# Kernel tuning notes

Measured on AMD Instinct MI355X. Metric: run time of the kernel, lower is better.

The kernel has to match this reference:

```python
import jax, jax.numpy as jnp
import numpy as np

C = 19
D = 128
TAU_HARD = 0.2
EMA = 0.999
BETA = 0.7
TH_I, TH_F = 0.5, 0.85
TL_I, TL_F = 0.1, 0.3
EPS = 1e-7


def _l2norm(x, axis):
    n = jnp.linalg.norm(x, axis=axis, keepdims=True)
    return x / jnp.maximum(n, 1e-12)


def _flatten_feat(feat):
    # [B,D,Hf,Wf] -> [N,D]
    B, Dd, Hf, Wf = feat.shape
    return feat.transpose(0, 2, 3, 1).reshape(-1, Dd)


def _build_protos(feat, labels, weights=None):
    # single-pass segment reduce replacing the per-class python loop
    f = _flatten_feat(feat)
    seg = labels.reshape(-1)
    w = jnp.ones(seg.shape, f.dtype) if weights is None else weights.reshape(-1)
    wsum_f = jax.ops.segment_sum(w[:, None] * f, seg, num_segments=C)  # [C,D]
    wsum = jax.ops.segment_sum(w, seg, num_segments=C)                 # [C]
    cnt = jax.ops.segment_sum(jnp.ones_like(w), seg, num_segments=C)
    proto = wsum_f / (wsum[:, None] + EPS)
    return proto, cnt >= 1.0


def _hard_contrastive(feat, labels, mem, mem_init):
    f = _l2norm(_flatten_feat(feat), axis=1)          # [N,D]
    lab = labels.reshape(-1)
    valid = mem_init[lab].astype(f.dtype)
    logits = (f @ mem.T) / TAU_HARD                   # [N,C]
    ce = -jnp.take_along_axis(jax.nn.log_softmax(logits, axis=1), lab[:, None], axis=1)[:, 0]
    nv = jnp.sum(valid)
    return jnp.where(nv > 0, jnp.sum(ce * valid) / jnp.maximum(nv, 1.0), 0.0)


def _ce_map(logits, target):
    # per-pixel cross entropy, logits [B,C,H,W], target [B,H,W]
    ls = jax.nn.log_softmax(logits, axis=1)
    return -jnp.take_along_axis(ls, target[:, None], axis=1)[:, 0]


def setup_inputs() -> dict:
    key = jax.random.key(0)
    ks = jax.random.split(key, 9)
    B, Hf, Wf = 4, 128, 128
    H = W = 512
    f = lambda k: jax.random.normal(k, (B, D, Hf, Wf), jnp.float32)
    g = lambda k: jax.random.normal(k, (B, C, H, W), jnp.float32)
    return {
        "feat_l1": f(ks[0]), "feat_l2": f(ks[1]),
        "feat_u1": f(ks[2]), "feat_u2": f(ks[3]),
        "logits_l1": g(ks[4]), "logits_l2": g(ks[5]),
        "logits_u1": g(ks[6]), "logits_u2": g(ks[7]),
        "memory": jnp.zeros((C, D), jnp.float32),
        "gt_labels": jax.random.randint(ks[8], (B, H, W), 0, C),
        "memory_init": jnp.zeros((C,), bool),
        "cur_iter": 10000,
        "max_iter": 40000,
    }


def reference(feat_l1, feat_l2, feat_u1, feat_u2, logits_l1, logits_l2,
              logits_u1, logits_u2, memory, gt_labels, memory_init,
              cur_iter, max_iter):
    B, _, Hf, Wf = feat_l1.shape
    H, W = logits_u1.shape[2], logits_u1.shape[3]

    q_u1 = jax.nn.softmax(logits_u1, axis=1)
    q_u2 = jax.nn.softmax(logits_u2, axis=1)

    # reliability r_u [B,H,W]
    y1 = jnp.argmax(q_u1, axis=1)
    y2 = jnp.argmax(q_u2, axis=1)
    agree = (y1 == y2).astype(q_u1.dtype)
    conf = (jnp.max(q_u1, axis=1) + jnp.max(q_u2, axis=1)) / 2.0
    m = (q_u1 + q_u2) / 2.0
    logm = jnp.log(jnp.maximum(m, EPS))
    kl1 = jnp.sum(q_u1 * (jnp.log(jnp.maximum(q_u1, EPS)) - logm), axis=1)
    kl2 = jnp.sum(q_u2 * (jnp.log(jnp.maximum(q_u2, EPS)) - logm), axis=1)
    r_u = agree * conf * jnp.exp(-(kl1 + kl2) / 2.0)

    # cosine-annealed thresholds
    ratio = float(cur_iter) / max(int(max_iter), 1)
    tau_high = TH_F - (TH_F - TH_I) * np.cos(np.pi * ratio / 2)

    # UCPS (pseudo labels are argmax of logits == argmax of softmax)
    loss_ucps = jnp.mean(jax.lax.stop_gradient(r_u) * (_ce_map(logits_u1, y2) + _ce_map(logits_u2, y1)))

    # nearest downsample (integer stride, matches torch nearest floor indexing)
    ih = jnp.arange(Hf) * (H // Hf)
    iw = jnp.arange(Wf) * (W // Wf)
    gt_down = gt_labels[:, ih][:, :, iw]
    pseudo_consensus = jnp.where(y1 != y2, 0, y1)
    pseudo_u_down = pseudo_consensus[:, ih][:, :, iw]
    # bilinear (align_corners=False == half-pixel, no antialias)
    r_u_down = jax.image.resize(r_u, (B, Hf, Wf), method='linear', antialias=False)

    anchor_mask = r_u_down > tau_high

    feat_l = (feat_l1 + feat_l2) / 2.0
    feat_u = (feat_u1 + feat_u2) / 2.0
    pl, pl_pres = _build_protos(feat_l, gt_down)
    anchor_r = jnp.where(anchor_mask, r_u_down, 0.0)
    pu, pu_pres = _build_protos(feat_u, pseudo_u_down, anchor_r)

    both = pl_pres & pu_pres
    merged = jnp.where(both[:, None], BETA * pl + (1.0 - BETA) * pu,
                       jnp.where(pl_pres[:, None], pl, pu))
    present = pl_pres | pu_pres
    merged = jax.lax.stop_gradient(merged)  # update_memory is no_grad

    p_norm = _l2norm(merged, axis=1)
    ema = _l2norm(EMA * memory + (1.0 - EMA) * p_norm, axis=1)
    new_mem = jnp.where((present & ~memory_init)[:, None], p_norm,
                        jnp.where((present & memory_init)[:, None], ema, memory))
    new_init = memory_init | present
    new_mem = jax.lax.stop_gradient(new_mem)

    loss_hard_l = (_hard_contrastive(feat_l1, gt_down, new_mem, new_init)
                   + _hard_contrastive(feat_l2, gt_down, new_mem, new_init)) / 2.0
    # contrastive_mode == 'all_hard'
    loss_hard_u = (_hard_contrastive(feat_u1, pseudo_u_down, new_mem, new_init)
                   + _hard_contrastive(feat_u2, pseudo_u_down, new_mem, new_init)) / 2.0

    loss_dgpc = loss_hard_l + loss_hard_u  # loss_soft == 0 in all_hard mode
    return jnp.stack([loss_dgpc, loss_ucps])
```

## Files before the change

kernel.cpp:

```cpp
#include <hip/hip_runtime.h>
#include <math.h>

#define NCLS 19
#define DD   128
#define EPSV 1e-7f
#define LOGEPS -16.118095651f

#define OFF_TAU    0
#define OFF_CNTL   8
#define OFF_WSUMU  32
#define OFF_CNTU   64
#define OFF_CE     96
#define OFF_VALID  100
#define OFF_UCPS   104
#define OFF_SUML   128
#define OFF_SUMU   2560
#define OFF_MEM    4992
#define OFF_INIT   7424
#define OFF_RUD    7456
#define OFF_PSEUDO 72992
#define ZERO_N     72992

__device__ __forceinline__ void fatom(float* p, float v) { unsafeAtomicAdd(p, v); }

__global__ __launch_bounds__(256) void kZ(float* __restrict__ W,
                                          const int* __restrict__ cur_it,
                                          const int* __restrict__ max_it) {
    int i = blockIdx.x * 256 + threadIdx.x;
    if (i == 0) {
        int mi = max_it[0]; if (mi < 1) mi = 1;
        double ratio = (double)cur_it[0] / (double)mi;
        W[OFF_TAU] = (float)(0.85 - (0.85 - 0.5) * cos(M_PI * ratio * 0.5));
    } else if (i < ZERO_N) {
        W[i] = 0.0f;
    }
}

__global__ __launch_bounds__(256, 2) void kB(const float* __restrict__ lu1,
                                             const float* __restrict__ lu2,
                                             float* __restrict__ W) {
    float* rud = W + OFF_RUD;
    int* pseudo = (int*)(W + OFF_PSEUDO);
    int t = blockIdx.x * 256 + threadIdx.x;
    int b = t >> 16;
    int rem4 = (t << 2) & 262143;
    int h = rem4 >> 9, w0 = rem4 & 511;

    const float4* p1 = (const float4*)lu1 + (size_t)b * (NCLS * 65536) + (rem4 >> 2);
    const float4* p2 = (const float4*)lu2 + (size_t)b * (NCLS * 65536) + (rem4 >> 2);

    float4 v1[NCLS], v2[NCLS];
#pragma unroll
    for (int c = 0; c < NCLS; c++) v1[c] = p1[c * 65536];
#pragma unroll
    for (int c = 0; c < NCLS; c++) v2[c] = p2[c * 65536];
    const float* a1 = (const float*)v1;
    const float* a2 = (const float*)v2;

    float contrib = 0.f;
    float ru12 = 0.f;
    int pl0 = 0;

#pragma unroll
    for (int e = 0; e < 4; e++) {
        float m1 = a1[e]; int y1 = 0;
        float m2 = a2[e]; int y2 = 0;
#pragma unroll
        for (int c = 1; c < NCLS; c++) {
            float x1 = a1[c * 4 + e], x2 = a2[c * 4 + e];
            if (x1 > m1) { m1 = x1; y1 = c; }
            if (x2 > m2) { m2 = x2; y2 = c; }
        }
        float s1 = 0.f, s2 = 0.f;
#pragma unroll
        for (int c = 0; c < NCLS; c++) {
            s1 += __expf(a1[c * 4 + e] - m1);
            s2 += __expf(a2[c * 4 + e] - m2);
        }
        float lse1 = m1 + __logf(s1);
        float lse2 = m2 + __logf(s2);

        float kl = 0.f, l1y2 = a1[e], l2y1 = a2[e];
#pragma unroll
        for (int c = 0; c < NCLS; c++) {
            float x1 = a1[c * 4 + e], x2 = a2[c * 4 + e];
            float lq1 = x1 - lse1, lq2 = x2 - lse2;
            float q1 = __expf(lq1), q2 = __expf(lq2);
            float mm = 0.5f * (q1 + q2);
            float lm = __logf(fmaxf(mm, EPSV));
            kl += q1 * (fmaxf(lq1, LOGEPS) - lm) + q2 * (fmaxf(lq2, LOGEPS) - lm);
            if (c == y2) l1y2 = x1;
            if (c == y1) l2y1 = x2;
        }
        float conf = 0.5f * (1.f / s1 + 1.f / s2);
        float r_u = (y1 == y2) ? conf * __expf(-0.5f * kl) : 0.f;
        float ce = (lse1 - l1y2) + (lse2 - l2y1);
        contrib += r_u * ce;
        if (e == 1 || e == 2) ru12 += r_u;
        if (e == 0) pl0 = (y1 == y2) ? y1 : 0;
    }

    float cs = contrib;
#pragma unroll
    for (int o = 32; o > 0; o >>= 1) cs += __shfl_down(cs, o, 64);
    __shared__ float wsum[4];
    if ((threadIdx.x & 63) == 0) wsum[threadIdx.x >> 6] = cs;
    __syncthreads();
    if (threadIdx.x == 0) fatom(&W[OFF_UCPS], wsum[0] + wsum[1] + wsum[2] + wsum[3]);

    int hm = h & 3;
    int didx = b * 16384 + (h >> 2) * 128 + (w0 >> 2);
    if (hm == 1 || hm == 2) fatom(&rud[didx], 0.25f * ru12);
    if (hm == 0) pseudo[didx] = pl0;
}

__global__ __launch_bounds__(256) void kC(const float* __restrict__ fl1,
                                          const float* __restrict__ fl2,
                                          const float* __restrict__ fu1,
                                          const float* __restrict__ fu2,
                                          const int* __restrict__ gt,
                                          float* __restrict__ W) {
    __shared__ float tile[DD * 33];
    __shared__ float accL[2 * NCLS * DD];
    __shared__ int   sLab[32], sCu[32];
    __shared__ float sW[32];
    __shared__ float sCntL[NCLS], sCntU[NCLS], sWUs[NCLS];

    int tid = threadIdx.x;
    for (int i = tid; i < 2 * NCLS * DD; i += 256) accL[i] = 0.f;
    if (tid < NCLS) { sCntL[tid] = 0.f; sCntU[tid] = 0.f; sWUs[tid] = 0.f; }
    __syncthreads();

    int P0 = blockIdx.x * 128;
    int b = P0 >> 14;
    const float tau = W[OFF_TAU];
    const float* rud = W + OFF_RUD;
    const int* pseudo = (const int*)(W + OFF_PSEUDO);
    size_t gb = (size_t)b * 2097152;

    int d = tid & 127, pg = tid >> 7;

    for (int T = 0; T < 4; T++) {
        int rem0 = (P0 + T * 32) & 16383;
        if (tid < 32) {
            int rem = rem0 + tid;
            int bp = b * 16384 + rem;
            int ii = rem >> 7, jj = rem & 127;
            int cl = gt[b * 262144 + ii * 2048 + jj * 4];
            int cu = pseudo[bp];
            float rd = rud[bp];
            float w = (rd > tau) ? rd : 0.f;
            sLab[tid] = cl; sCu[tid] = cu; sW[tid] = w;
            fatom(&sCntL[cl], 1.f);
            fatom(&sCntU[cu], 1.f);
            if (w > 0.f) fatom(&sWUs[cu], w);
        }
        for (int i = tid; i < 1024; i += 256) {
            int dd = i >> 3, p4 = (i & 7) << 2;
            size_t g = gb + (size_t)dd * 16384 + rem0 + p4;
            float4 x1 = *(const float4*)(fl1 + g);
            float4 x2 = *(const float4*)(fl2 + g);
            float* tp = &tile[dd * 33 + p4];
            tp[0] = 0.5f * (x1.x + x2.x);
            tp[1] = 0.5f * (x1.y + x2.y);
            tp[2] = 0.5f * (x1.z + x2.z);
            tp[3] = 0.5f * (x1.w + x2.w);
        }
        __syncthreads();
        float* aL = &accL[pg * (NCLS * DD) + d];
#pragma unroll
        for (int p = pg * 16; p < pg * 16 + 16; p++) {
            int c = sLab[p];
            aL[c * DD] += tile[d * 33 + p];
            float w = sW[p];
            if (w > 0.f) {
                size_t g = gb + (size_t)d * 16384 + rem0 + p;
                fatom(&W[OFF_SUMU + sCu[p] * DD + d], w * 0.5f * (fu1[g] + fu2[g]));
            }
        }
        __syncthreads();
    }
    for (int i = tid; i < NCLS * DD; i += 256)
        fatom(&W[OFF_SUML + i], accL[i] + accL[NCLS * DD + i]);
    if (tid < NCLS) {
        fatom(&W[OFF_CNTL + tid], sCntL[tid]);
        fatom(&W[OFF_WSUMU + tid], sWUs[tid]);
        fatom(&W[OFF_CNTU + tid], sCntU[tid]);
    }
}

__global__ __launch_bounds__(128) void kD(const float* __restrict__ mem,
                                          const unsigned char* __restrict__ minit,
                                          float* __restrict__ W) {
    int c = blockIdx.x, d = threadIdx.x;
    __shared__ float red[128];
    float cntL = W[OFF_CNTL + c], wsU = W[OFF_WSUMU + c], cntU = W[OFF_CNTU + c];
    bool plp = cntL >= 1.f, pup = cntU >= 1.f;
    float pl = W[OFF_SUML + c * DD + d] / (cntL + EPSV);
    float pu = W[OFF_SUMU + c * DD + d] / (wsU + EPSV);
    float merged = (plp && pup) ? (0.7f * pl + 0.3f * pu) : (plp ? pl : pu);

    red[d] = merged * merged; __syncthreads();
    for (int s = 64; s > 0; s >>= 1) { if (d < s) red[d] += red[d + s]; __syncthreads(); }
    float nrm = red[0];
    __syncthreads();
    float pn = merged / fmaxf(sqrtf(nrm), 1e-12f);

    float mo = mem[c * DD + d];
    float e = 0.999f * mo + 0.001f * pn;
    red[d] = e * e; __syncthreads();
    for (int s = 64; s > 0; s >>= 1) { if (d < s) red[d] += red[d + s]; __syncthreads(); }
    float ne = red[0];
    float ema = e / fmaxf(sqrtf(ne), 1e-12f);

    bool present = plp || pup;
    bool init = (minit[c] != 0);
    float nm = present ? (init ? ema : pn) : mo;
    W[OFF_MEM + c * DD + d] = nm;
    if (d == 0) W[OFF_INIT + c] = (init || present) ? 1.f : 0.f;
}

__device__ __forceinline__ void pix_loss(const float dots[NCLS], float nn, int lab,
                                         const float* sInit, float& ce_acc, float& v_acc) {
    float inv = 5.0f / fmaxf(sqrtf(nn), 1e-12f);
    float lg[NCLS];
#pragma unroll
    for (int c = 0; c < NCLS; c++) lg[c] = dots[c] * inv;
    float mx = lg[0];
#pragma unroll
    for (int c = 1; c < NCLS; c++) mx = fmaxf(mx, lg[c]);
    float s = 0.f;
#pragma unroll
    for (int c = 0; c < NCLS; c++) s += __expf(lg[c] - mx);
    float lse = mx + __logf(s);
    float ll = lg[0];
#pragma unroll
    for (int c = 1; c < NCLS; c++) if (c == lab) ll = lg[c];
    float vld = sInit[lab];
    ce_acc += vld * (lse - ll);
    v_acc += vld;
}

__global__ __launch_bounds__(256) void kE(const float* __restrict__ f0,
                                          const float* __restrict__ f1,
                                          const float* __restrict__ f2,
                                          const float* __restrict__ f3,
                                          const int* __restrict__ gt,
                                          float* __restrict__ W) {
    __shared__ __align__(16) float sMem[NCLS * DD];
    __shared__ float sInit[NCLS];
    __shared__ float redA[256], redB[256];
    int fid = blockIdx.y;
    const float* feat = (fid == 0) ? f0 : (fid == 1) ? f1 : (fid == 2) ? f2 : f3;
    for (int i = threadIdx.x; i < NCLS * DD; i += 256) sMem[i] = W[OFF_MEM + i];
    if (threadIdx.x < NCLS) sInit[threadIdx.x] = W[OFF_INIT + threadIdx.x];
    __syncthreads();

    int p0 = blockIdx.x * 512 + threadIdx.x;
    int b = p0 >> 14;
    int rem0 = p0 & 16383;
    const float* fp = feat + (size_t)b * 2097152 + rem0;

    float dots0[NCLS], dots1[NCLS];
#pragma unroll
    for (int c = 0; c < NCLS; c++) { dots0[c] = 0.f; dots1[c] = 0.f; }
    float n0 = 0.f, n1 = 0.f;

    for (int d0 = 0; d0 < DD; d0 += 8) {
        const float* fpp = fp + (size_t)d0 * 16384;
        float a[8], bb[8];
#pragma unroll
        for (int j = 0; j < 8; j++) {
            a[j]  = fpp[(size_t)j * 16384];
            bb[j] = fpp[(size_t)j * 16384 + 256];
        }
#pragma unroll
        for (int j = 0; j < 8; j++) { n0 += a[j] * a[j]; n1 += bb[j] * bb[j]; }
#pragma unroll
        for (int c = 0; c < NCLS; c++) {
            float4 m0 = *(const float4*)&sMem[c * DD + d0];
            float4 m1 = *(const float4*)&sMem[c * DD + d0 + 4];
            dots0[c] += a[0] * m0.x + a[1] * m0.y + a[2] * m0.z + a[3] * m0.w
                      + a[4] * m1.x + a[5] * m1.y + a[6] * m1.z + a[7] * m1.w;
            dots1[c] += bb[0] * m0.x + bb[1] * m0.y + bb[2] * m0.z + bb[3] * m0.w
                      + bb[4] * m1.x + bb[5] * m1.y + bb[6] * m1.z + bb[7] * m1.w;
        }
    }

    const int* pseudo = (const int*)(W + OFF_PSEUDO);
    int rem1 = rem0 + 256;
    int lab0 = (fid < 2) ? gt[b * 262144 + (rem0 >> 7) * 2048 + (rem0 & 127) * 4] : pseudo[p0];
    int lab1 = (fid < 2) ? gt[b * 262144 + (rem1 >> 7) * 2048 + (rem1 & 127) * 4] : pseudo[p0 + 256];

    float ce_acc = 0.f, v_acc = 0.f;
    pix_loss(dots0, n0, lab0, sInit, ce_acc, v_acc);
    pix_loss(dots1, n1, lab1, sInit, ce_acc, v_acc);

    redA[threadIdx.x] = ce_acc;
    redB[threadIdx.x] = v_acc;
    __syncthreads();
    for (int s = 128; s > 0; s >>= 1) {
        if (threadIdx.x < s) { redA[threadIdx.x] += redA[threadIdx.x + s]; redB[threadIdx.x] += redB[threadIdx.x + s]; }
        __syncthreads();
    }
    if (threadIdx.x == 0) {
        fatom(&W[OFF_CE + fid], redA[0]);
        fatom(&W[OFF_VALID + fid], redB[0]);
    }
}

__global__ void kF(float* __restrict__ out, const float* __restrict__ W) {
    if (threadIdx.x == 0 && blockIdx.x == 0) {
        float h[4];
#pragma unroll
        for (int i = 0; i < 4; i++) {
            float nv = W[OFF_VALID + i];
            h[i] = (nv > 0.f) ? W[OFF_CE + i] / fmaxf(nv, 1.f) : 0.f;
        }
        out[0] = 0.5f * (h[0] + h[1]) + 0.5f * (h[2] + h[3]);
        out[1] = W[OFF_UCPS] * (1.0f / 1048576.0f);
    }
}

extern "C" void kernel_launch(void* const* d_in, const int* in_sizes, int n_in,
                              void* d_out, int out_size, void* d_ws, size_t ws_size,
                              hipStream_t stream) {
    const float* fl1 = (const float*)d_in[0];
    const float* fl2 = (const float*)d_in[1];
    const float* fu1 = (const float*)d_in[2];
    const float* fu2 = (const float*)d_in[3];
    const float* lu1 = (const float*)d_in[6];
    const float* lu2 = (const float*)d_in[7];
    const float* mem = (const float*)d_in[8];
    const int* gt = (const int*)d_in[9];
    const unsigned char* minit = (const unsigned char*)d_in[10];
    const int* cur = (const int*)d_in[11];
    const int* mxi = (const int*)d_in[12];
    float* W = (float*)d_ws;
    float* out = (float*)d_out;

    kZ<<<286, 256, 0, stream>>>(W, cur, mxi);
    kB<<<1024, 256, 0, stream>>>(lu1, lu2, W);
    kC<<<512, 256, 0, stream>>>(fl1, fl2, fu1, fu2, gt, W);
    kD<<<NCLS, 128, 0, stream>>>(mem, minit, W);
    kE<<<dim3(128, 4), 256, 0, stream>>>(fl1, fl2, fu1, fu2, gt, W);
    kF<<<1, 64, 0, stream>>>(out, W);
}
```

Baseline: 418.1 us.

## Stage unsupervised logits through LDS and process one pixel per thread

```diff
diff --git a/kernel.cpp b/kernel.cpp
--- a/kernel.cpp
+++ b/kernel.cpp
@@ -36,82 +36,76 @@
     }
 }
 
-__global__ __launch_bounds__(256, 2) void kB(const float* __restrict__ lu1,
-                                             const float* __restrict__ lu2,
-                                             float* __restrict__ W) {
+__global__ __launch_bounds__(256) void kB(const float* __restrict__ lu1,
+                                          const float* __restrict__ lu2,
+                                          float* __restrict__ W) {
+    __shared__ float sA[NCLS * 256];
+    __shared__ float sB[NCLS * 256];
+    __shared__ float wsum[4];
+
     float* rud = W + OFF_RUD;
     int* pseudo = (int*)(W + OFF_PSEUDO);
-    int t = blockIdx.x * 256 + threadIdx.x;
-    int b = t >> 16;
-    int rem4 = (t << 2) & 262143;
-    int h = rem4 >> 9, w0 = rem4 & 511;
-
-    const float4* p1 = (const float4*)lu1 + (size_t)b * (NCLS * 65536) + (rem4 >> 2);
-    const float4* p2 = (const float4*)lu2 + (size_t)b * (NCLS * 65536) + (rem4 >> 2);
-
-    float4 v1[NCLS], v2[NCLS];
-#pragma unroll
-    for (int c = 0; c < NCLS; c++) v1[c] = p1[c * 65536];
-#pragma unroll
-    for (int c = 0; c < NCLS; c++) v2[c] = p2[c * 65536];
-    const float* a1 = (const float*)v1;
-    const float* a2 = (const float*)v2;
-
-    float contrib = 0.f;
-    float ru12 = 0.f;
-    int pl0 = 0;
-
-#pragma unroll
-    for (int e = 0; e < 4; e++) {
-        float m1 = a1[e]; int y1 = 0;
-        float m2 = a2[e]; int y2 = 0;
-#pragma unroll
-        for (int c = 1; c < NCLS; c++) {
-            float x1 = a1[c * 4 + e], x2 = a2[c * 4 + e];
-            if (x1 > m1) { m1 = x1; y1 = c; }
-            if (x2 > m2) { m2 = x2; y2 = c; }
-        }
-        float s1 = 0.f, s2 = 0.f;
-#pragma unroll
-        for (int c = 0; c < NCLS; c++) {
-            s1 += __expf(a1[c * 4 + e] - m1);
-            s2 += __expf(a2[c * 4 + e] - m2);
-        }
-        float lse1 = m1 + __logf(s1);
-        float lse2 = m2 + __logf(s2);
-
-        float kl = 0.f, l1y2 = a1[e], l2y1 = a2[e];
-#pragma unroll
-        for (int c = 0; c < NCLS; c++) {
-            float x1 = a1[c * 4 + e], x2 = a2[c * 4 + e];
-            float lq1 = x1 - lse1, lq2 = x2 - lse2;
-            float q1 = __expf(lq1), q2 = __expf(lq2);
-            float mm = 0.5f * (q1 + q2);
-            float lm = __logf(fmaxf(mm, EPSV));
-            kl += q1 * (fmaxf(lq1, LOGEPS) - lm) + q2 * (fmaxf(lq2, LOGEPS) - lm);
-            if (c == y2) l1y2 = x1;
-            if (c == y1) l2y1 = x2;
-        }
-        float conf = 0.5f * (1.f / s1 + 1.f / s2);
-        float r_u = (y1 == y2) ? conf * __expf(-0.5f * kl) : 0.f;
-        float ce = (lse1 - l1y2) + (lse2 - l2y1);
-        contrib += r_u * ce;
-        if (e == 1 || e == 2) ru12 += r_u;
-        if (e == 0) pl0 = (y1 == y2) ? y1 : 0;
-    }
-
-    float cs = contrib;
-#pragma unroll
-    for (int o = 32; o > 0; o >>= 1) cs += __shfl_down(cs, o, 64);
-    __shared__ float wsum[4];
-    if ((threadIdx.x & 63) == 0) wsum[threadIdx.x >> 6] = cs;
-    __syncthreads();
-    if (threadIdx.x == 0) fatom(&W[OFF_UCPS], wsum[0] + wsum[1] + wsum[2] + wsum[3]);
-
-    int hm = h & 3;
-    int didx = b * 16384 + (h >> 2) * 128 + (w0 >> 2);
-    if (hm == 1 || hm == 2) fatom(&rud[didx], 0.25f * ru12);
-    if (hm == 0) pseudo[didx] = pl0;
+    int tid = threadIdx.x;
+    int b = blockIdx.x >> 10;
+    int rem_base = (blockIdx.x & 1023) << 8;
+
+    {
+        const float4* g1 = (const float4*)lu1 + (size_t)b * (NCLS * 65536) + (rem_base >> 2);
+        const float4* g2 = (const float4*)lu2 + (size_t)b * (NCLS * 65536) + (rem_base >> 2);
+        float4* d1 = (float4*)sA;
+        float4* d2 = (float4*)sB;
+        for (int i = tid; i < NCLS * 64; i += 256) {
+            int c = i >> 6, e = i & 63;
+            d1[c * 64 + e] = g1[c * 65536 + e];
+            d2[c * 64 + e] = g2[c * 65536 + e];
+        }
+    }
+    __syncthreads();
+
+    float m1, m2, l1y2, l2y1;
+    int y1 = 0, y2 = 0;
+    m1 = sA[tid]; m2 = sB[tid];
+    l2y1 = m2;    l1y2 = m1;
+#pragma unroll
+    for (int c = 1; c < NCLS; c++) {
+        float x1 = sA[c * 256 + tid], x2 = sB[c * 256 + tid];
+        if (x1 > m1) { m1 = x1; y1 = c; l2y1 = x2; }
+        if (x2 > m2) { m2 = x2; y2 = c; l1y2 = x1; }
+    }
+    float s1 = 0.f, s2 = 0.f;
+#pragma unroll
+    for (int c = 0; c < NCLS; c++) {
+        s1 += __expf(sA[c * 256 + tid] - m1);
+        s2 += __expf(sB[c * 256 + tid] - m2);
+    }
+    float lse1 = m1 + __logf(s1);
+    float lse2 = m2 + __logf(s2);
+    float kl = 0.f;
+#pragma unroll
+    for (int c = 0; c < NCLS; c++) {
+        float lq1 = sA[c * 256 + tid] - lse1, lq2 = sB[c * 256 + tid] - lse2;
+        float q1 = __expf(lq1), q2 = __expf(lq2);
+        float mm = 0.5f * (q1 + q2);
+        float lm = __logf(fmaxf(mm, EPSV));
+        kl += q1 * (fmaxf(lq1, LOGEPS) - lm) + q2 * (fmaxf(lq2, LOGEPS) - lm);
+    }
+    float conf = 0.5f * (1.f / s1 + 1.f / s2);
+    float r_u = (y1 == y2) ? conf * __expf(-0.5f * kl) : 0.f;
+    float ce = (lse1 - l1y2) + (lse2 - l2y1);
+    float contrib = r_u * ce;
+
+#pragma unroll
+    for (int o = 32; o > 0; o >>= 1) contrib += __shfl_down(contrib, o, 64);
+    if ((tid & 63) == 0) wsum[tid >> 6] = contrib;
+    __syncthreads();
+    if (tid == 0) fatom(&W[OFF_UCPS], wsum[0] + wsum[1] + wsum[2] + wsum[3]);
+
+    int rem = rem_base + tid;
+    int h = rem >> 9, w = rem & 511;
+    int hm = h & 3, wm = w & 3;
+    int didx = b * 16384 + (h >> 2) * 128 + (w >> 2);
+    if ((hm == 1 || hm == 2) && (wm == 1 || wm == 2)) fatom(&rud[didx], 0.25f * r_u);
+    if (hm == 0 && wm == 0) pseudo[didx] = (y1 == y2) ? y1 : 0;
 }
 
 __global__ __launch_bounds__(256) void kC(const float* __restrict__ fl1,
@@ -340,7 +334,7 @@
     float* out = (float*)d_out;
 
     kZ<<<286, 256, 0, stream>>>(W, cur, mxi);
-    kB<<<1024, 256, 0, stream>>>(lu1, lu2, W);
+    kB<<<4096, 256, 0, stream>>>(lu1, lu2, W);
     kC<<<512, 256, 0, stream>>>(fl1, fl2, fu1, fu2, gt, W);
     kD<<<NCLS, 128, 0, stream>>>(mem, minit, W);
     kE<<<dim3(128, 4), 256, 0, stream>>>(fl1, fl2, fu1, fu2, gt, W);
```

Result: slower. 429.4 us (+2.7%).
